# Kernel optimization log

Measured on AMD Instinct MI355X. Metric: run time of the kernel, lower is better.

The kernel has to match this reference:

```python
import jax, jax.numpy as jnp
import numpy as np

D_INNER, D_STATE, DT_RANK = 2048, 16, 128
BATCH, SEQ = 2, 2048


def setup_inputs() -> dict:
    key = jax.random.key(0)
    ks = jax.random.split(key, 6)
    x = jax.random.normal(ks[0], (BATCH, SEQ, D_INNER), dtype=jnp.float32)
    # A_log initialized uniform(-4, -1) per _init_parameters
    A_log = jax.random.uniform(ks[1], (D_INNER, D_STATE), minval=-4.0, maxval=-1.0, dtype=jnp.float32)
    D = jnp.ones((D_INNER,), dtype=jnp.float32)
    # torch Linear weights: [out_features, in_features], kaiming-uniform-ish scale
    x_proj_w = jax.random.normal(ks[2], (DT_RANK + 2 * D_STATE, D_INNER), dtype=jnp.float32) / np.sqrt(D_INNER)
    dt_proj_w = jax.random.normal(ks[3], (D_INNER, DT_RANK), dtype=jnp.float32) / np.sqrt(DT_RANK)
    dt_std = DT_RANK ** (-0.5)
    dt_proj_b = jax.random.uniform(ks[4], (D_INNER,), minval=-dt_std, maxval=dt_std, dtype=jnp.float32)
    return {"x": x, "A_log": A_log, "D": D, "x_proj_w": x_proj_w,
            "dt_proj_w": dt_proj_w, "dt_proj_b": dt_proj_b}


def _selective_scan(u, delta, A, B, C, D):
    # u, delta: [b, l, d]; A: [d, n]; B, C: [b, l, n]; D: [d]
    dA = jnp.exp(delta[..., None] * A[None, None])          # [b, l, d, n]
    dBu = (delta * u)[..., None] * B[:, :, None, :]         # [b, l, d, n]

    def step(h, inp):
        dA_t, dBu_t, C_t = inp                              # [b,d,n],[b,d,n],[b,n]
        h = dA_t * h + dBu_t
        y_t = jnp.einsum('bdn,bn->bd', h, C_t)
        return h, y_t

    h0 = jnp.zeros((u.shape[0], u.shape[2], A.shape[1]), dtype=u.dtype)
    xs = (jnp.moveaxis(dA, 1, 0), jnp.moveaxis(dBu, 1, 0), jnp.moveaxis(C, 1, 0))
    _, ys = jax.lax.scan(step, h0, xs)                      # ys: [l, b, d]
    y = jnp.moveaxis(ys, 0, 1)
    return y + u * D[None, None, :]


def reference(x, A_log, D, x_proj_w, dt_proj_w, dt_proj_b):
    # x: [b, l, d_inner]
    x_dbl = jnp.einsum('bld,ed->ble', x, x_proj_w)          # [b, l, dt_rank + 2n]
    delta_r = x_dbl[..., :DT_RANK]
    B = x_dbl[..., DT_RANK:DT_RANK + D_STATE]
    C = x_dbl[..., DT_RANK + D_STATE:]
    delta = jnp.einsum('blr,dr->bld', delta_r, dt_proj_w) + dt_proj_b
    delta = jax.nn.softplus(delta)                          # delta_softplus=True
    A = -jnp.exp(A_log)
    return _selective_scan(x, delta, A, B, C, D)
```

## Files before the change

### kernel.cpp

```cpp
#include <hip/hip_runtime.h>
#include <hip/hip_bf16.h>
#include <math.h>

#define DI   2048
#define DS   16
#define DTR  128
#define NBATCH 2
#define SEQ  2048
#define ROWS (NBATCH*SEQ)
#define NE   (DTR + 2*DS)
#define NC   64
#define LC   (SEQ/NC)

typedef float f32x4 __attribute__((ext_vector_type(4)));
typedef short s16x8 __attribute__((ext_vector_type(8)));
typedef short s16x4 __attribute__((ext_vector_type(4)));

__device__ inline short f2bf(float f) {
    unsigned u = __builtin_bit_cast(unsigned, f);
    u += 0x7FFFu + ((u >> 16) & 1u);
    return (short)(u >> 16);
}

__device__ inline unsigned pk2(float lo, float hi) {
    union { __hip_bfloat162 h; unsigned u; } cv;
    cv.h = __float22bfloat162_rn(float2{lo, hi});
    return cv.u;
}
__device__ inline unsigned packdu(short dbf, float xf) {
    return ((unsigned)(unsigned short)f2bf(xf) << 16) | (unsigned)(unsigned short)dbf;
}

__global__ __launch_bounds__(256) void k_castw(const float* __restrict__ w,
                                               const float* __restrict__ dtw,
                                               short* __restrict__ wb,
                                               short* __restrict__ dtwb) {
    int i = blockIdx.x*256 + threadIdx.x;
    if (i < 81920) {
        float4 v = ((const float4*)w)[i];
        s16x4 o = { f2bf(v.x), f2bf(v.y), f2bf(v.z), f2bf(v.w) };
        *(s16x4*)(wb + 4*i) = o;
    } else if (i < 147456) {
        int j = i - 81920;
        float4 v = ((const float4*)dtw)[j];
        s16x4 o = { f2bf(v.x), f2bf(v.y), f2bf(v.z), f2bf(v.w) };
        *(s16x4*)(dtwb + 4*j) = o;
    }
}

__global__ __launch_bounds__(256) void k_gemm1(const float* __restrict__ x,
                                               const short* __restrict__ wb,
                                               short* __restrict__ dRb,
                                               float* __restrict__ Bm,
                                               float* __restrict__ Cm) {
    const int wave = blockIdx.x*4 + (threadIdx.x >> 6);
    const int lane = threadIdx.x & 63;
    const int m16  = wave & 255;
    const int half = wave >> 8;
    const int r = lane & 15, g = lane >> 4;
    f32x4 acc[5];
    #pragma unroll
    for (int i = 0; i < 5; i++) acc[i] = (f32x4){0.f,0.f,0.f,0.f};

    const float* xp = x + (size_t)(m16*16 + r)*DI + g*8;
    const short* wbase = wb + (size_t)(half*80 + r)*DI + g*8;
    #pragma unroll 2
    for (int kk = 0; kk < 64; ++kk) {
        const int k0 = kk*32;
        float4 xa = *(const float4*)(xp + k0);
        float4 xc = *(const float4*)(xp + k0 + 4);
        union { s16x8 v; unsigned u[4]; } af;
        af.u[0] = pk2(xa.x, xa.y);
        af.u[1] = pk2(xa.z, xa.w);
        af.u[2] = pk2(xc.x, xc.y);
        af.u[3] = pk2(xc.z, xc.w);
        #pragma unroll
        for (int nf = 0; nf < 5; ++nf) {
            s16x8 bfrag = *(const s16x8*)(wbase + (size_t)nf*16*DI + k0);
            acc[nf] = __builtin_amdgcn_mfma_f32_16x16x32_bf16(af.v, bfrag, acc[nf], 0, 0, 0);
        }
    }
    const int orow = m16*16 + g*4;
    #pragma unroll
    for (int nf = 0; nf < 5; ++nf) {
        const int gnf = half*5 + nf;
        const int col = gnf*16 + r;
        #pragma unroll
        for (int j = 0; j < 4; ++j) {
            const int row = orow + j;
            float v = acc[nf][j];
            if (gnf < 8)       dRb[(size_t)row*DTR + col]        = f2bf(v);
            else if (gnf == 8) Bm [(size_t)row*DS + (col - 128)] = v;
            else               Cm [(size_t)row*DS + (col - 144)] = v;
        }
    }
}

__global__ __launch_bounds__(256) void k_gemm2(const short* __restrict__ dRb,
                                               const short* __restrict__ dtwb,
                                               const float* __restrict__ bias,
                                               unsigned short* __restrict__ deltab) {
    const int wave = blockIdx.x*4 + (threadIdx.x >> 6);
    const int lane = threadIdx.x & 63;
    const int m16 = wave >> 5, nt = wave & 31;
    const int r = lane & 15, g = lane >> 4;

    s16x8 a[4];
    const short* ap = dRb + (size_t)(m16*16 + r)*DTR + g*8;
    #pragma unroll
    for (int ks = 0; ks < 4; ++ks) a[ks] = *(const s16x8*)(ap + ks*32);

    f32x4 acc[4];
    #pragma unroll
    for (int i = 0; i < 4; i++) acc[i] = (f32x4){0.f,0.f,0.f,0.f};

    #pragma unroll
    for (int nf = 0; nf < 4; ++nf) {
        const short* bp = dtwb + (size_t)(nt*64 + nf*16 + r)*DTR + g*8;
        #pragma unroll
        for (int ks = 0; ks < 4; ++ks) {
            s16x8 b = *(const s16x8*)(bp + ks*32);
            acc[nf] = __builtin_amdgcn_mfma_f32_16x16x32_bf16(a[ks], b, acc[nf], 0, 0, 0);
        }
    }
    const int orow = m16*16 + g*4;
    #pragma unroll
    for (int nf = 0; nf < 4; ++nf) {
        const int col = nt*64 + nf*16 + r;
        const float bb = bias[col];
        #pragma unroll
        for (int j = 0; j < 4; ++j) {
            float v = acc[nf][j] + bb;
            float sp = fmaxf(v, 0.f) + __logf(1.f + __expf(-fabsf(v)));
            deltab[(size_t)(orow + j)*DI + col] = (unsigned short)f2bf(sp);
        }
    }
}

__global__ __launch_bounds__(256) void k_scan1(const unsigned short* __restrict__ deltab,
                                               const float* __restrict__ x,
                                               const float* __restrict__ Bm,
                                               const float* __restrict__ A_log,
                                               float* __restrict__ aprod,
                                               float* __restrict__ rsum) {
    __shared__ unsigned lxd[LC][64];
    __shared__ float lB[LC][DS];
    const int tid = threadIdx.x;
    const int bb = blockIdx.x & 31;
    const int b  = (blockIdx.x >> 5) & 1;
    const int c  = blockIdx.x >> 6;
    const int d0 = bb*64;
    const int lbase = c*LC;

    {
        const unsigned short* dsrc = deltab + ((size_t)(b*SEQ + lbase))*DI + d0;
        const float*          xsrc = x      + ((size_t)(b*SEQ + lbase))*DI + d0;
        const int row = tid >> 4, col = (tid & 15)*4;
        #pragma unroll
        for (int i = 0; i < 2; i++) {
            s16x4  dv = *(const s16x4*) (dsrc + (size_t)(row + 16*i)*DI + col);
            float4 xv = *(const float4*)(xsrc + (size_t)(row + 16*i)*DI + col);
            uint4 o;
            o.x = packdu(dv[0], xv.x);
            o.y = packdu(dv[1], xv.y);
            o.z = packdu(dv[2], xv.z);
            o.w = packdu(dv[3], xv.w);
            *(uint4*)&lxd[row + 16*i][col] = o;
        }
        if (tid < 128) {
            const float* bsrc = Bm + ((size_t)(b*SEQ + lbase))*DS;
            *(float4*)&lB[tid >> 2][(tid & 3)*4] = *(const float4*)(bsrc + tid*4);
        }
    }

    const int lane = tid & 63, widx = tid >> 6;
    const int dlow = lane & 15, q = lane >> 4;
    const int dcol = widx*16 + dlow;
    const int d = d0 + dcol;
    const int n0 = 4*q;

    float4 Alg = *(const float4*)(A_log + (size_t)d*DS + n0);
    float An[4] = { -__expf(Alg.x), -__expf(Alg.y), -__expf(Alg.z), -__expf(Alg.w) };
    float r[4] = {0.f,0.f,0.f,0.f};
    float S = 0.f;

    __syncthreads();

    #pragma unroll 8
    for (int tt = 0; tt < LC; ++tt) {
        unsigned v = lxd[tt][dcol];
        float dlt = __builtin_bit_cast(float, v << 16);
        float u   = __builtin_bit_cast(float, v & 0xffff0000u);
        float du  = dlt * u;
        S += dlt;
        float4 bv = *(const float4*)&lB[tt][n0];
        float bbv[4] = {bv.x, bv.y, bv.z, bv.w};
        #pragma unroll
        for (int j = 0; j < 4; ++j) {
            float da = __expf(dlt * An[j]);
            r[j] = fmaf(da, r[j], du * bbv[j]);
        }
    }
    size_t base = (((size_t)c*NBATCH + b)*DI + d)*DS + n0;
    *(float4*)(aprod + base) = (float4){ __expf(An[0]*S), __expf(An[1]*S),
                                         __expf(An[2]*S), __expf(An[3]*S) };
    *(float4*)(rsum  + base) = (float4){ r[0], r[1], r[2], r[3] };
}

__global__ __launch_bounds__(256) void k_mid(float* ah,
                                             const float* __restrict__ rsum) {
    int gid = blockIdx.x*256 + threadIdx.x;
    int n = gid & 15;
    int d = (gid >> 4) & (DI-1);
    int b = gid >> 15;
    float h = 0.f;
    for (int c = 0; c < NC; c++) {
        size_t idx = (((size_t)c*NBATCH + b)*DI + d)*DS + n;
        float a  = ah[idx];
        float rr = rsum[idx];
        ah[idx] = h;
        h = fmaf(a, h, rr);
    }
}

__global__ __launch_bounds__(256) void k_scan2(const unsigned short* __restrict__ deltab,
                                               const float* __restrict__ x,
                                               const float* __restrict__ Bm,
                                               const float* __restrict__ Cm,
                                               const float* __restrict__ A_log,
                                               const float* __restrict__ Dv,
                                               const float* __restrict__ hin,
                                               float* __restrict__ y) {
    __shared__ unsigned lxd[LC][64];
    __shared__ float lB[LC][DS];
    __shared__ float lC[LC][DS];
    const int tid = threadIdx.x;
    const int bb = blockIdx.x & 31;
    const int b  = (blockIdx.x >> 5) & 1;
    const int c  = blockIdx.x >> 6;
    const int d0 = bb*64;
    const int lbase = c*LC;

    {
        const unsigned short* dsrc = deltab + ((size_t)(b*SEQ + lbase))*DI + d0;
        const float*          xsrc = x      + ((size_t)(b*SEQ + lbase))*DI + d0;
        const int row = tid >> 4, col = (tid & 15)*4;
        #pragma unroll
        for (int i = 0; i < 2; i++) {
            s16x4  dv = *(const s16x4*) (dsrc + (size_t)(row + 16*i)*DI + col);
            float4 xv = *(const float4*)(xsrc + (size_t)(row + 16*i)*DI + col);
            uint4 o;
            o.x = packdu(dv[0], xv.x);
            o.y = packdu(dv[1], xv.y);
            o.z = packdu(dv[2], xv.z);
            o.w = packdu(dv[3], xv.w);
            *(uint4*)&lxd[row + 16*i][col] = o;
        }
        if (tid < 128) {
            const float* bsrc = Bm + ((size_t)(b*SEQ + lbase))*DS;
            const float* csrc = Cm + ((size_t)(b*SEQ + lbase))*DS;
            *(float4*)&lB[tid >> 2][(tid & 3)*4] = *(const float4*)(bsrc + tid*4);
            *(float4*)&lC[tid >> 2][(tid & 3)*4] = *(const float4*)(csrc + tid*4);
        }
    }

    const int lane = tid & 63, widx = tid >> 6;
    const int dlow = lane & 15, q = lane >> 4;
    const int dcol = widx*16 + dlow;
    const int d = d0 + dcol;
    const int n0 = 4*q;

    float4 Alg = *(const float4*)(A_log + (size_t)d*DS + n0);
    float An[4] = { -__expf(Alg.x), -__expf(Alg.y), -__expf(Alg.z), -__expf(Alg.w) };
    size_t base = (((size_t)c*NBATCH + b)*DI + d)*DS + n0;
    float4 hv = *(const float4*)(hin + base);
    float h[4] = {hv.x, hv.y, hv.z, hv.w};
    const float Dd = Dv[d];
    float* yp = y + ((size_t)(b*SEQ + lbase))*DI + d;

    __syncthreads();

    #pragma unroll 8
    for (int tt = 0; tt < LC; ++tt) {
        unsigned v = lxd[tt][dcol];
        float dlt = __builtin_bit_cast(float, v << 16);
        float u   = __builtin_bit_cast(float, v & 0xffff0000u);
        float du  = dlt * u;
        float4 bv = *(const float4*)&lB[tt][n0];
        float4 cv = *(const float4*)&lC[tt][n0];
        float bbv[4] = {bv.x, bv.y, bv.z, bv.w};
        float ccv[4] = {cv.x, cv.y, cv.z, cv.w};
        float acc = 0.f;
        #pragma unroll
        for (int j = 0; j < 4; ++j) {
            float da = __expf(dlt * An[j]);
            h[j] = fmaf(da, h[j], du * bbv[j]);
            acc  = fmaf(h[j], ccv[j], acc);
        }
        acc += __shfl_xor(acc, 16);
        acc += __shfl_xor(acc, 32);
        if (q == 0) yp[(size_t)tt*DI] = fmaf(u, Dd, acc);
    }
}

extern "C" void kernel_launch(void* const* d_in, const int* in_sizes, int n_in,
                              void* d_out, int out_size, void* d_ws, size_t ws_size,
                              hipStream_t stream) {
    const float* x     = (const float*)d_in[0];
    const float* A_log = (const float*)d_in[1];
    const float* Dv    = (const float*)d_in[2];
    const float* xpw   = (const float*)d_in[3];
    const float* dtw   = (const float*)d_in[4];
    const float* dtb   = (const float*)d_in[5];
    float* out = (float*)d_out;

    const size_t SCN = (size_t)NC*NBATCH*DS*DI;

    float* ws    = (float*)d_ws;
    unsigned short* deltab = (unsigned short*)ws;
    float* aprod = ws + ((size_t)ROWS*DI/2);
    float* rsum  = aprod + SCN;
    float* Bm    = rsum + SCN;
    float* Cm    = Bm + (size_t)ROWS*DS;
    short* dRb   = (short*)(Cm + (size_t)ROWS*DS);
    short* wb    = dRb + (size_t)ROWS*DTR;
    short* dtwb  = wb  + (size_t)160*2048;

    k_castw<<<576, 256, 0, stream>>>(xpw, dtw, wb, dtwb);
    k_gemm1<<<128, 256, 0, stream>>>(x, wb, dRb, Bm, Cm);
    k_gemm2<<<2048, 256, 0, stream>>>(dRb, dtwb, dtb, deltab);
    k_scan1<<<4096, 256, 0, stream>>>(deltab, x, Bm, A_log, aprod, rsum);
    k_mid<<<256, 256, 0, stream>>>(aprod, rsum);
    k_scan2<<<4096, 256, 0, stream>>>(deltab, x, Bm, Cm, A_log, Dv, aprod, out);
}
```

Baseline: 228.5 us.

## Split-K gemm1 across waves, parallelize chunk-carry scan, use exp2 in scans

```diff
diff --git a/kernel.cpp b/kernel.cpp
--- a/kernel.cpp
+++ b/kernel.cpp
@@ -15,6 +15,8 @@
 typedef float f32x4 __attribute__((ext_vector_type(4)));
 typedef short s16x8 __attribute__((ext_vector_type(8)));
 typedef short s16x4 __attribute__((ext_vector_type(4)));
+
+#define L2E 1.4426950408889634f
 
 __device__ inline short f2bf(float f) {
     unsigned u = __builtin_bit_cast(unsigned, f);
@@ -48,24 +50,24 @@
     }
 }
 
-__global__ __launch_bounds__(256) void k_gemm1(const float* __restrict__ x,
+__global__ __launch_bounds__(512) void k_gemm1(const float* __restrict__ x,
                                                const short* __restrict__ wb,
                                                short* __restrict__ dRb,
                                                float* __restrict__ Bm,
                                                float* __restrict__ Cm) {
-    const int wave = blockIdx.x*4 + (threadIdx.x >> 6);
-    const int lane = threadIdx.x & 63;
-    const int m16  = wave & 255;
-    const int half = wave >> 8;
+    __shared__ float lred[2][3][5][64][4];
+    const int tid  = threadIdx.x;
+    const int w    = tid >> 6;
+    const int lane = tid & 63;
+    const int half = w & 1, kq = w >> 1;
+    const int m16  = blockIdx.x;
     const int r = lane & 15, g = lane >> 4;
-    f32x4 acc[5];
-    #pragma unroll
-    for (int i = 0; i < 5; i++) acc[i] = (f32x4){0.f,0.f,0.f,0.f};
-
-    const float* xp = x + (size_t)(m16*16 + r)*DI + g*8;
-    const short* wbase = wb + (size_t)(half*80 + r)*DI + g*8;
-    #pragma unroll 2
-    for (int kk = 0; kk < 64; ++kk) {
+
+    f32x4 acc[5] = {};
+    const float* xp    = x  + (size_t)(m16*16 + r)*DI + g*8 + kq*512;
+    const short* wbase = wb + (size_t)(half*80 + r)*DI + g*8 + kq*512;
+    #pragma unroll 4
+    for (int kk = 0; kk < 16; ++kk) {
         const int k0 = kk*32;
         float4 xa = *(const float4*)(xp + k0);
         float4 xc = *(const float4*)(xp + k0 + 4);
@@ -80,18 +82,31 @@
             acc[nf] = __builtin_amdgcn_mfma_f32_16x16x32_bf16(af.v, bfrag, acc[nf], 0, 0, 0);
         }
     }
-    const int orow = m16*16 + g*4;
-    #pragma unroll
-    for (int nf = 0; nf < 5; ++nf) {
-        const int gnf = half*5 + nf;
-        const int col = gnf*16 + r;
-        #pragma unroll
-        for (int j = 0; j < 4; ++j) {
-            const int row = orow + j;
-            float v = acc[nf][j];
-            if (gnf < 8)       dRb[(size_t)row*DTR + col]        = f2bf(v);
-            else if (gnf == 8) Bm [(size_t)row*DS + (col - 128)] = v;
-            else               Cm [(size_t)row*DS + (col - 144)] = v;
+    if (kq > 0) {
+        #pragma unroll
+        for (int nf = 0; nf < 5; ++nf)
+            *(f32x4*)&lred[half][kq-1][nf][lane][0] = acc[nf];
+    }
+    __syncthreads();
+    if (kq == 0) {
+        #pragma unroll
+        for (int nf = 0; nf < 5; ++nf)
+            #pragma unroll
+            for (int p = 0; p < 3; ++p)
+                acc[nf] += *(const f32x4*)&lred[half][p][nf][lane][0];
+        const int orow = m16*16 + g*4;
+        #pragma unroll
+        for (int nf = 0; nf < 5; ++nf) {
+            const int gnf = half*5 + nf;
+            const int col = gnf*16 + r;
+            #pragma unroll
+            for (int j = 0; j < 4; ++j) {
+                const int row = orow + j;
+                float v = acc[nf][j];
+                if (gnf < 8)       dRb[(size_t)row*DTR + col]        = f2bf(v);
+                else if (gnf == 8) Bm [(size_t)row*DS + (col - 128)] = v;
+                else               Cm [(size_t)row*DS + (col - 144)] = v;
+            }
         }
     }
 }
@@ -110,10 +125,7 @@
     #pragma unroll
     for (int ks = 0; ks < 4; ++ks) a[ks] = *(const s16x8*)(ap + ks*32);
 
-    f32x4 acc[4];
-    #pragma unroll
-    for (int i = 0; i < 4; i++) acc[i] = (f32x4){0.f,0.f,0.f,0.f};
-
+    f32x4 acc[4] = {};
     #pragma unroll
     for (int nf = 0; nf < 4; ++nf) {
         const short* bp = dtwb + (size_t)(nt*64 + nf*16 + r)*DTR + g*8;
@@ -180,7 +192,8 @@
     const int n0 = 4*q;
 
     float4 Alg = *(const float4*)(A_log + (size_t)d*DS + n0);
-    float An[4] = { -__expf(Alg.x), -__expf(Alg.y), -__expf(Alg.z), -__expf(Alg.w) };
+    float An2[4] = { -__expf(Alg.x)*L2E, -__expf(Alg.y)*L2E,
+                     -__expf(Alg.z)*L2E, -__expf(Alg.w)*L2E };
     float r[4] = {0.f,0.f,0.f,0.f};
     float S = 0.f;
 
@@ -197,29 +210,49 @@
         float bbv[4] = {bv.x, bv.y, bv.z, bv.w};
         #pragma unroll
         for (int j = 0; j < 4; ++j) {
-            float da = __expf(dlt * An[j]);
+            float da = exp2f(An2[j] * dlt);
             r[j] = fmaf(da, r[j], du * bbv[j]);
         }
     }
     size_t base = (((size_t)c*NBATCH + b)*DI + d)*DS + n0;
-    *(float4*)(aprod + base) = (float4){ __expf(An[0]*S), __expf(An[1]*S),
-                                         __expf(An[2]*S), __expf(An[3]*S) };
-    *(float4*)(rsum  + base) = (float4){ r[0], r[1], r[2], r[3] };
-}
-
-__global__ __launch_bounds__(256) void k_mid(float* ah,
+    *(f32x4*)(aprod + base) = (f32x4){ exp2f(An2[0]*S), exp2f(An2[1]*S),
+                                       exp2f(An2[2]*S), exp2f(An2[3]*S) };
+    *(f32x4*)(rsum  + base) = (f32x4){ r[0], r[1], r[2], r[3] };
+}
+
+__global__ __launch_bounds__(256) void k_mid(float* __restrict__ ah,
                                              const float* __restrict__ rsum) {
-    int gid = blockIdx.x*256 + threadIdx.x;
-    int n = gid & 15;
-    int d = (gid >> 4) & (DI-1);
-    int b = gid >> 15;
+    __shared__ float lA[8][32];
+    __shared__ float lR[8][32];
+    const int tid = threadIdx.x;
+    const int s  = tid >> 5;
+    const int el = tid & 31;
+    const size_t E = (size_t)NBATCH*DI*DS;
+    const size_t e = (size_t)blockIdx.x*32 + el;
+
+    float a[8], r[8];
+    #pragma unroll
+    for (int i = 0; i < 8; ++i) {
+        size_t idx = (size_t)(s*8 + i)*E + e;
+        a[i] = ah[idx];
+        r[i] = rsum[idx];
+    }
+    float A = 1.f, R = 0.f;
+    #pragma unroll
+    for (int i = 0; i < 8; ++i) {
+        A = a[i]*A;
+        R = fmaf(a[i], R, r[i]);
+    }
+    lA[s][el] = A; lR[s][el] = R;
+    __syncthreads();
     float h = 0.f;
-    for (int c = 0; c < NC; c++) {
-        size_t idx = (((size_t)c*NBATCH + b)*DI + d)*DS + n;
-        float a  = ah[idx];
-        float rr = rsum[idx];
+    for (int k = 0; k < s; ++k)
+        h = fmaf(lA[k][el], h, lR[k][el]);
+    #pragma unroll
+    for (int i = 0; i < 8; ++i) {
+        size_t idx = (size_t)(s*8 + i)*E + e;
         ah[idx] = h;
-        h = fmaf(a, h, rr);
+        h = fmaf(a[i], h, r[i]);
     }
 }
 
@@ -271,7 +304,8 @@
     const int n0 = 4*q;
 
     float4 Alg = *(const float4*)(A_log + (size_t)d*DS + n0);
-    float An[4] = { -__expf(Alg.x), -__expf(Alg.y), -__expf(Alg.z), -__expf(Alg.w) };
+    float An2[4] = { -__expf(Alg.x)*L2E, -__expf(Alg.y)*L2E,
+                     -__expf(Alg.z)*L2E, -__expf(Alg.w)*L2E };
     size_t base = (((size_t)c*NBATCH + b)*DI + d)*DS + n0;
     float4 hv = *(const float4*)(hin + base);
     float h[4] = {hv.x, hv.y, hv.z, hv.w};
@@ -293,7 +327,7 @@
         float acc = 0.f;
         #pragma unroll
         for (int j = 0; j < 4; ++j) {
-            float da = __expf(dlt * An[j]);
+            float da = exp2f(An2[j] * dlt);
             h[j] = fmaf(da, h[j], du * bbv[j]);
             acc  = fmaf(h[j], ccv[j], acc);
         }
@@ -327,9 +361,9 @@
     short* dtwb  = wb  + (size_t)160*2048;
 
     k_castw<<<576, 256, 0, stream>>>(xpw, dtw, wb, dtwb);
-    k_gemm1<<<128, 256, 0, stream>>>(x, wb, dRb, Bm, Cm);
+    k_gemm1<<<256, 512, 0, stream>>>(x, wb, dRb, Bm, Cm);
     k_gemm2<<<2048, 256, 0, stream>>>(dRb, dtwb, dtb, deltab);
     k_scan1<<<4096, 256, 0, stream>>>(deltab, x, Bm, A_log, aprod, rsum);
-    k_mid<<<256, 256, 0, stream>>>(aprod, rsum);
+    k_mid<<<2048, 256, 0, stream>>>(aprod, rsum);
     k_scan2<<<4096, 256, 0, stream>>>(deltab, x, Bm, Cm, A_log, Dv, aprod, out);
 }
```

Result: no change. 230.3 us (+0.8%).
